# Performance work log

Hardware: AMD Instinct MI355X
Metric: run time of the kernel (lower is better)

The kernel has to match this reference:

```python
import jax, jax.numpy as jnp
import numpy as np

# module hyperparameters (from init_kwargs)
STRIDE, PAD, DIL = 1, 1, 1
GROUPS, DG = 1, 1
KH, KW = 3, 3
CIN, COUT = 256, 256


def _mdcn_forward(x, offset, mask, weight, bias):
    B, C, H, W = x.shape
    Cout = weight.shape[0]
    K = KH * KW
    Ho = (H + 2 * PAD - (DIL * (KH - 1) + 1)) // STRIDE + 1
    Wo = (W + 2 * PAD - (DIL * (KW - 1) + 1)) // STRIDE + 1
    Cg = C // DG

    # offset channel layout: ((g*K + k)*2 + {0: dy, 1: dx})
    off = offset.reshape(B, DG, KH, KW, 2, Ho, Wo)
    base_y = (jnp.arange(Ho) * STRIDE - PAD)[None, :] + DIL * jnp.arange(KH)[:, None]  # [KH,Ho]
    base_x = (jnp.arange(Wo) * STRIDE - PAD)[None, :] + DIL * jnp.arange(KW)[:, None]  # [KW,Wo]
    sy = base_y[None, None, :, None, :, None].astype(x.dtype) + off[:, :, :, :, 0]  # [B,DG,KH,KW,Ho,Wo]
    sx = base_x[None, None, None, :, None, :].astype(x.dtype) + off[:, :, :, :, 1]

    y0f = jnp.floor(sy); x0f = jnp.floor(sx)
    wy = sy - y0f; wx = sx - x0f
    y0 = y0f.astype(jnp.int32); x0 = x0f.astype(jnp.int32)

    xg = x.reshape(B, DG, Cg, H * W)

    def corner(yc, xc, w):
        valid = (yc >= 0) & (yc < H) & (xc >= 0) & (xc < W)
        idx = jnp.clip(yc, 0, H - 1) * W + jnp.clip(xc, 0, W - 1)  # [B,DG,KH,KW,Ho,Wo]
        v = jnp.take_along_axis(xg, idx.reshape(B, DG, 1, -1), axis=3)  # [B,DG,Cg,K*Ho*Wo]
        v = v.reshape(B, DG, Cg, KH, KW, Ho, Wo)
        return v * (w * valid.astype(x.dtype))[:, :, None]

    val = (corner(y0, x0, (1 - wy) * (1 - wx))
           + corner(y0, x0 + 1, (1 - wy) * wx)
           + corner(y0 + 1, x0, wy * (1 - wx))
           + corner(y0 + 1, x0 + 1, wy * wx))  # [B,DG,Cg,KH,KW,Ho,Wo]

    cols = val * mask.reshape(B, DG, 1, KH, KW, Ho, Wo)
    cols = cols.reshape(B, GROUPS, (C // GROUPS) * K, Ho * Wo)
    wg = weight.reshape(GROUPS, Cout // GROUPS, (C // GROUPS) * K)
    out = jnp.einsum('gok,bgkp->bgop', wg, cols).reshape(B, Cout, Ho, Wo)
    return out + bias[None, :, None, None]


def setup_inputs() -> dict:
    key = jax.random.key(0)
    k1, k2, k3, k4 = jax.random.split(key, 4)
    B, H, W = 4, 64, 64
    x = jax.random.normal(k1, (B, CIN, H, W), dtype=jnp.float32)
    offset = jax.random.normal(k2, (B, 2 * DG * KH * KW, H, W), dtype=jnp.float32)
    mask = jax.random.uniform(k3, (B, DG * KH * KW, H, W), dtype=jnp.float32)
    stdv = 1.0 / np.sqrt(CIN * KH * KW)
    weight = jax.random.uniform(k4, (COUT, CIN // GROUPS, KH, KW), dtype=jnp.float32,
                                minval=-stdv, maxval=stdv)
    bias = jnp.zeros((COUT,), dtype=jnp.float32)
    return {"x": x, "offset": offset, "mask": mask, "weight": weight, "bias": bias}


def reference(x, offset, mask, weight, bias):
    return _mdcn_forward(x, offset, mask, weight, bias)
```

## Files before the change

kernel.cpp:

```cpp
#include <hip/hip_runtime.h>
#include <hip/hip_bf16.h>
#include <stdint.h>

#define KDIM 2304

typedef __bf16 bf16_t;
typedef bf16_t bf16x8 __attribute__((ext_vector_type(8)));
typedef float f32x4 __attribute__((ext_vector_type(4)));
typedef float f32x2 __attribute__((ext_vector_type(2)));

__device__ __forceinline__ float b2f_lo(uint32_t u) {
  union { uint32_t i; float f; } c; c.i = u << 16; return c.f;
}
__device__ __forceinline__ float b2f_hi(uint32_t u) {
  union { uint32_t i; float f; } c; c.i = u & 0xffff0000u; return c.f;
}
__device__ __forceinline__ uint32_t pk_bf16(float a, float b) {
  __hip_bfloat162 h = __float22bfloat162_rn(make_float2(a, b));
  union { __hip_bfloat162 h; uint32_t u; } c; c.h = h; return c.u;
}

__device__ __forceinline__ void g2lds16(const uint16_t* g, uint16_t* l) {
  __builtin_amdgcn_global_load_lds((const __attribute__((address_space(1))) void*)g,
                                   (__attribute__((address_space(3))) void*)l,
                                   16, 0, 0);
}

__global__ __launch_bounds__(256) void k_transpose(const float* __restrict__ x,
                                                   uint16_t* __restrict__ xt) {
  __shared__ float tile[32][33];
  int b = blockIdx.z;
  int c0 = blockIdx.y << 5;
  int s0 = blockIdx.x << 5;
  int tid = threadIdx.x;
  int tx = tid & 31, ty = tid >> 5;
  const float* src = x + ((size_t)(b * 256 + c0)) * 4096 + s0;
#pragma unroll
  for (int i = 0; i < 4; ++i)
    tile[ty + i * 8][tx] = src[(size_t)(ty + i * 8) * 4096 + tx];
  __syncthreads();
  int cg = tid & 7, sp = tid >> 3;
  uint2 o;
  o.x = pk_bf16(tile[cg * 4 + 0][sp], tile[cg * 4 + 1][sp]);
  o.y = pk_bf16(tile[cg * 4 + 2][sp], tile[cg * 4 + 3][sp]);
  *(uint2*)&xt[((size_t)b * 4096 + s0 + sp) * 256 + c0 + cg * 4] = o;
}

__global__ __launch_bounds__(256) void k_wprep(const float* __restrict__ w,
                                               uint16_t* __restrict__ wt) {
  int t = blockIdx.x * 256 + threadIdx.x;
  int cout = t / KDIM;
  int r = t - cout * KDIM;
  int k = r >> 8, c = r & 255;
  wt[t] = (uint16_t)(pk_bf16(w[((size_t)(cout * 256 + c)) * 9 + k], 0.f) & 0xffffu);
}

#define BM 128
#define BN 64
#define BK 32
__global__ __launch_bounds__(256) void k_fused(const uint16_t* __restrict__ xt,
                                               const uint16_t* __restrict__ A,
                                               const float* __restrict__ off,
                                               const float* __restrict__ msk,
                                               const float* __restrict__ bias,
                                               float* __restrict__ out) {
  __shared__ __align__(16) uint16_t As[BM * BK];
  __shared__ __align__(16) uint16_t Bs[BN * BK];
  __shared__ float s_off[18 * 64];
  __shared__ float s_msk[9 * 64];

  int tid = threadIdx.x;
  int n0 = blockIdx.x << 6;
  int m0 = blockIdx.y << 7;
  int b = blockIdx.x >> 6;
  int ho = blockIdx.x & 63;

  const float* offb = off + (size_t)b * 18 * 4096 + ho * 64;
  for (int i = tid; i < 18 * 64; i += 256)
    s_off[i] = offb[(size_t)(i >> 6) * 4096 + (i & 63)];
  const float* mskb = msk + (size_t)b * 9 * 4096 + ho * 64;
  for (int i = tid; i < 9 * 64; i += 256)
    s_msk[i] = mskb[(size_t)(i >> 6) * 4096 + (i & 63)];
  __syncthreads();

  int lane = tid & 63, wv = tid >> 6;
  int wm = wv >> 1, wn = wv & 1;
  int q = lane >> 4, r = lane & 15;

  f32x4 acc[4][2];
#pragma unroll
  for (int i = 0; i < 4; ++i)
#pragma unroll
    for (int j = 0; j < 2; ++j) acc[i][j] = f32x4{0.f, 0.f, 0.f, 0.f};

  const uint16_t* a0p = A + (size_t)(m0 + (tid >> 2)) * KDIM + (tid & 3) * 8;
  const uint16_t* a1p = A + (size_t)(m0 + 64 + (tid >> 2)) * KDIM + (tid & 3) * 8;
  uint16_t* as0 = &As[tid * 8];
  uint16_t* as1 = &As[2048 + tid * 8];

  int p = tid >> 2, cq = tid & 3;
  uint16_t* bs_dst = &Bs[tid * 8];
  const uint16_t* xtb = xt + (size_t)b * 4096 * 256 + cq * 8;

  for (int tap = 0; tap < 9; ++tap) {
    int kh = tap / 3, kw = tap - kh * 3;
    float dy = s_off[(2 * tap) * 64 + p];
    float dx = s_off[(2 * tap + 1) * 64 + p];
    float mm = s_msk[tap * 64 + p];
    float sy = (float)(ho - 1 + kh) + dy;
    float sx = (float)(p - 1 + kw) + dx;
    float fy = floorf(sy), fx = floorf(sx);
    int y0 = (int)fy, x0 = (int)fx;
    float wy = sy - fy, wx = sx - fx;
    float cw[4];
    const uint16_t* cp[4];
#pragma unroll
    for (int cy = 0; cy < 2; ++cy) {
#pragma unroll
      for (int cx = 0; cx < 2; ++cx) {
        int y = y0 + cy, x = x0 + cx;
        float w = (cy ? wy : 1.f - wy) * (cx ? wx : 1.f - wx) * mm;
        bool v = ((unsigned)y < 64u) && ((unsigned)x < 64u);
        w = v ? w : 0.f;
        int yc = min(max(y, 0), 63), xc = min(max(x, 0), 63);
        cw[cy * 2 + cx] = w;
        cp[cy * 2 + cx] = xtb + ((yc << 6) + xc) * 256;
      }
    }
    const uint16_t* abase0 = a0p + tap * 256;
    const uint16_t* abase1 = a1p + tap * 256;
#pragma unroll
    for (int st = 0; st < 8; ++st) {
      g2lds16(abase0 + st * 32, as0);
      g2lds16(abase1 + st * 32, as1);
      const uint4 d0 = *(const uint4*)(cp[0] + st * 32);
      const uint4 d1 = *(const uint4*)(cp[1] + st * 32);
      const uint4 d2 = *(const uint4*)(cp[2] + st * 32);
      const uint4 d3 = *(const uint4*)(cp[3] + st * 32);
      f32x2 v0 = {0.f, 0.f}, v1 = {0.f, 0.f}, v2 = {0.f, 0.f}, v3 = {0.f, 0.f};
      f32x2 w0 = {cw[0], cw[0]}, w1 = {cw[1], cw[1]}, w2 = {cw[2], cw[2]}, w3 = {cw[3], cw[3]};
      v0 += w0 * f32x2{b2f_lo(d0.x), b2f_hi(d0.x)};
      v1 += w0 * f32x2{b2f_lo(d0.y), b2f_hi(d0.y)};
      v2 += w0 * f32x2{b2f_lo(d0.z), b2f_hi(d0.z)};
      v3 += w0 * f32x2{b2f_lo(d0.w), b2f_hi(d0.w)};
      v0 += w1 * f32x2{b2f_lo(d1.x), b2f_hi(d1.x)};
      v1 += w1 * f32x2{b2f_lo(d1.y), b2f_hi(d1.y)};
      v2 += w1 * f32x2{b2f_lo(d1.z), b2f_hi(d1.z)};
      v3 += w1 * f32x2{b2f_lo(d1.w), b2f_hi(d1.w)};
      v0 += w2 * f32x2{b2f_lo(d2.x), b2f_hi(d2.x)};
      v1 += w2 * f32x2{b2f_lo(d2.y), b2f_hi(d2.y)};
      v2 += w2 * f32x2{b2f_lo(d2.z), b2f_hi(d2.z)};
      v3 += w2 * f32x2{b2f_lo(d2.w), b2f_hi(d2.w)};
      v0 += w3 * f32x2{b2f_lo(d3.x), b2f_hi(d3.x)};
      v1 += w3 * f32x2{b2f_lo(d3.y), b2f_hi(d3.y)};
      v2 += w3 * f32x2{b2f_lo(d3.z), b2f_hi(d3.z)};
      v3 += w3 * f32x2{b2f_lo(d3.w), b2f_hi(d3.w)};
      uint4 o;
      o.x = pk_bf16(v0.x, v0.y);
      o.y = pk_bf16(v1.x, v1.y);
      o.z = pk_bf16(v2.x, v2.y);
      o.w = pk_bf16(v3.x, v3.y);
      *(uint4*)bs_dst = o;
      __syncthreads();
      bf16x8 af[4], bfr[2];
#pragma unroll
      for (int mi = 0; mi < 4; ++mi)
        af[mi] = *(const bf16x8*)&As[(wm * 64 + mi * 16 + r) * BK + q * 8];
#pragma unroll
      for (int ni = 0; ni < 2; ++ni)
        bfr[ni] = *(const bf16x8*)&Bs[(wn * 32 + ni * 16 + r) * BK + q * 8];
#pragma unroll
      for (int mi = 0; mi < 4; ++mi)
#pragma unroll
        for (int ni = 0; ni < 2; ++ni)
          acc[mi][ni] = __builtin_amdgcn_mfma_f32_16x16x32_bf16(af[mi], bfr[ni], acc[mi][ni], 0, 0, 0);
      __syncthreads();
    }
  }

#pragma unroll
  for (int mi = 0; mi < 4; ++mi) {
#pragma unroll
    for (int j = 0; j < 4; ++j) {
      int m = m0 + wm * 64 + mi * 16 + q * 4 + j;
      float bv = bias[m];
#pragma unroll
      for (int ni = 0; ni < 2; ++ni) {
        int n = n0 + wn * 32 + ni * 16 + r;
        int bb = n >> 12, pp = n & 4095;
        out[((size_t)(bb * 256 + m)) * 4096 + pp] = acc[mi][ni][j] + bv;
      }
    }
  }
}

extern "C" void kernel_launch(void* const* d_in, const int* in_sizes, int n_in,
                              void* d_out, int out_size, void* d_ws, size_t ws_size,
                              hipStream_t stream) {
  (void)in_sizes; (void)n_in; (void)out_size; (void)ws_size;
  const float* x      = (const float*)d_in[0];
  const float* offset = (const float*)d_in[1];
  const float* mask   = (const float*)d_in[2];
  const float* weight = (const float*)d_in[3];
  const float* bias   = (const float*)d_in[4];
  float* out = (float*)d_out;

  uint8_t* ws = (uint8_t*)d_ws;
  uint16_t* xt = (uint16_t*)ws;
  uint16_t* wt = (uint16_t*)(ws + 8388608);

  k_transpose<<<dim3(128, 8, 4), 256, 0, stream>>>(x, xt);
  k_wprep<<<dim3(2304), 256, 0, stream>>>(weight, wt);
  k_fused<<<dim3(256, 2), 256, 0, stream>>>(xt, wt, offset, mask, bias, out);
}
```

Baseline: 142.5 us.

## Merge prep kernels and enlarge fused GEMM tile to 128x128 with K=128 stages

After: 178.8 us. 25.5% more time.

```diff
diff --git a/kernel.cpp b/kernel.cpp
--- a/kernel.cpp
+++ b/kernel.cpp
@@ -26,89 +26,98 @@
                                    16, 0, 0);
 }
 
-__global__ __launch_bounds__(256) void k_transpose(const float* __restrict__ x,
-                                                   uint16_t* __restrict__ xt) {
-  __shared__ float tile[32][33];
-  int b = blockIdx.z;
-  int c0 = blockIdx.y << 5;
-  int s0 = blockIdx.x << 5;
+__global__ __launch_bounds__(256) void k_prep(const float* __restrict__ x,
+                                              uint16_t* __restrict__ xt,
+                                              const float* __restrict__ w,
+                                              uint16_t* __restrict__ wt) {
   int tid = threadIdx.x;
-  int tx = tid & 31, ty = tid >> 5;
-  const float* src = x + ((size_t)(b * 256 + c0)) * 4096 + s0;
-#pragma unroll
-  for (int i = 0; i < 4; ++i)
-    tile[ty + i * 8][tx] = src[(size_t)(ty + i * 8) * 4096 + tx];
-  __syncthreads();
-  int cg = tid & 7, sp = tid >> 3;
-  uint2 o;
-  o.x = pk_bf16(tile[cg * 4 + 0][sp], tile[cg * 4 + 1][sp]);
-  o.y = pk_bf16(tile[cg * 4 + 2][sp], tile[cg * 4 + 3][sp]);
-  *(uint2*)&xt[((size_t)b * 4096 + s0 + sp) * 256 + c0 + cg * 4] = o;
-}
-
-__global__ __launch_bounds__(256) void k_wprep(const float* __restrict__ w,
-                                               uint16_t* __restrict__ wt) {
-  int t = blockIdx.x * 256 + threadIdx.x;
-  int cout = t / KDIM;
-  int r = t - cout * KDIM;
-  int k = r >> 8, c = r & 255;
-  wt[t] = (uint16_t)(pk_bf16(w[((size_t)(cout * 256 + c)) * 9 + k], 0.f) & 0xffffu);
-}
-
-#define BM 128
-#define BN 64
-#define BK 32
-__global__ __launch_bounds__(256) void k_fused(const uint16_t* __restrict__ xt,
-                                               const uint16_t* __restrict__ A,
-                                               const float* __restrict__ off,
-                                               const float* __restrict__ msk,
-                                               const float* __restrict__ bias,
-                                               float* __restrict__ out) {
-  __shared__ __align__(16) uint16_t As[BM * BK];
-  __shared__ __align__(16) uint16_t Bs[BN * BK];
-  __shared__ float s_off[18 * 64];
-  __shared__ float s_msk[9 * 64];
+  if (blockIdx.x < 2048) {
+    __shared__ float tile[32][65];
+    int b = blockIdx.x >> 9;
+    int cgrp = (blockIdx.x >> 6) & 7;
+    int sgrp = blockIdx.x & 63;
+    int c0 = cgrp << 5, s0 = sgrp << 6;
+#pragma unroll
+    for (int it = 0; it < 2; ++it) {
+      int f = tid + it * 256;
+      int r = f >> 4, col = (f & 15) << 2;
+      float4 v = *(const float4*)&x[((size_t)(b * 256 + c0 + r)) * 4096 + s0 + col];
+      tile[r][col + 0] = v.x;
+      tile[r][col + 1] = v.y;
+      tile[r][col + 2] = v.z;
+      tile[r][col + 3] = v.w;
+    }
+    __syncthreads();
+    int sp = tid >> 2, cg = tid & 3;
+    uint4 o;
+    o.x = pk_bf16(tile[cg * 8 + 0][sp], tile[cg * 8 + 1][sp]);
+    o.y = pk_bf16(tile[cg * 8 + 2][sp], tile[cg * 8 + 3][sp]);
+    o.z = pk_bf16(tile[cg * 8 + 4][sp], tile[cg * 8 + 5][sp]);
+    o.w = pk_bf16(tile[cg * 8 + 6][sp], tile[cg * 8 + 7][sp]);
+    *(uint4*)&xt[((size_t)b * 4096 + s0 + sp) * 256 + c0 + cg * 8] = o;
+  } else {
+    __shared__ float wl[2304];
+    int cout = blockIdx.x - 2048;
+    const float* wrow = w + (size_t)cout * 2304;
+    for (int i = tid; i < 576; i += 256)
+      *(float4*)&wl[i * 4] = *(const float4*)&wrow[i * 4];
+    __syncthreads();
+    uint16_t* wdst = wt + (size_t)cout * KDIM + tid;
+#pragma unroll
+    for (int t = 0; t < 9; ++t)
+      wdst[t * 256] = (uint16_t)(pk_bf16(wl[tid * 9 + t], 0.f) & 0xffffu);
+  }
+}
+
+__global__ __launch_bounds__(256, 1) void k_fused(const uint16_t* __restrict__ xt,
+                                                  const uint16_t* __restrict__ wt,
+                                                  const float* __restrict__ off,
+                                                  const float* __restrict__ msk,
+                                                  const float* __restrict__ bias,
+                                                  float* __restrict__ out) {
+  __shared__ __align__(16) uint16_t As[4][128][32];
+  __shared__ __align__(16) uint16_t Bs[4][128][32];
+  __shared__ float s_off[18 * 128];
+  __shared__ float s_msk[9 * 128];
 
   int tid = threadIdx.x;
-  int n0 = blockIdx.x << 6;
+  int b = blockIdx.x >> 5;
+  int hobase = (blockIdx.x & 31) << 1;
+  int n0 = b * 4096 + hobase * 64;
   int m0 = blockIdx.y << 7;
-  int b = blockIdx.x >> 6;
-  int ho = blockIdx.x & 63;
-
-  const float* offb = off + (size_t)b * 18 * 4096 + ho * 64;
-  for (int i = tid; i < 18 * 64; i += 256)
-    s_off[i] = offb[(size_t)(i >> 6) * 4096 + (i & 63)];
-  const float* mskb = msk + (size_t)b * 9 * 4096 + ho * 64;
-  for (int i = tid; i < 9 * 64; i += 256)
-    s_msk[i] = mskb[(size_t)(i >> 6) * 4096 + (i & 63)];
+
+  const float* offb = off + (size_t)b * 18 * 4096 + hobase * 64;
+  for (int i = tid; i < 18 * 128; i += 256)
+    s_off[i] = offb[(size_t)(i >> 7) * 4096 + (i & 127)];
+  const float* mskb = msk + (size_t)b * 9 * 4096 + hobase * 64;
+  for (int i = tid; i < 9 * 128; i += 256)
+    s_msk[i] = mskb[(size_t)(i >> 7) * 4096 + (i & 127)];
   __syncthreads();
 
   int lane = tid & 63, wv = tid >> 6;
   int wm = wv >> 1, wn = wv & 1;
   int q = lane >> 4, r = lane & 15;
 
-  f32x4 acc[4][2];
+  f32x4 acc[4][4];
 #pragma unroll
   for (int i = 0; i < 4; ++i)
 #pragma unroll
-    for (int j = 0; j < 2; ++j) acc[i][j] = f32x4{0.f, 0.f, 0.f, 0.f};
-
-  const uint16_t* a0p = A + (size_t)(m0 + (tid >> 2)) * KDIM + (tid & 3) * 8;
-  const uint16_t* a1p = A + (size_t)(m0 + 64 + (tid >> 2)) * KDIM + (tid & 3) * 8;
-  uint16_t* as0 = &As[tid * 8];
-  uint16_t* as1 = &As[2048 + tid * 8];
-
-  int p = tid >> 2, cq = tid & 3;
-  uint16_t* bs_dst = &Bs[tid * 8];
-  const uint16_t* xtb = xt + (size_t)b * 4096 * 256 + cq * 8;
+    for (int j = 0; j < 4; ++j) acc[i][j] = f32x4{0.f, 0.f, 0.f, 0.f};
+
+  const uint16_t* aptr = wt + (size_t)(m0 + (lane >> 2)) * KDIM + wv * 32 + (lane & 3) * 8;
+
+  int p = tid >> 1, half = tid & 1;
+  const uint16_t* xtb = xt + (size_t)b * 4096 * 256 + half * 64;
+  int ho_p = hobase + (p >> 6);
+  int wo_p = p & 63;
 
   for (int tap = 0; tap < 9; ++tap) {
     int kh = tap / 3, kw = tap - kh * 3;
-    float dy = s_off[(2 * tap) * 64 + p];
-    float dx = s_off[(2 * tap + 1) * 64 + p];
-    float mm = s_msk[tap * 64 + p];
-    float sy = (float)(ho - 1 + kh) + dy;
-    float sx = (float)(p - 1 + kw) + dx;
+    float dy = s_off[(2 * tap) * 128 + p];
+    float dx = s_off[(2 * tap + 1) * 128 + p];
+    float mm = s_msk[tap * 128 + p];
+    float sy = (float)(ho_p - 1 + kh) + dy;
+    float sx = (float)(wo_p - 1 + kw) + dx;
     float fy = floorf(sy), fx = floorf(sx);
     int y0 = (int)fy, x0 = (int)fx;
     float wy = sy - fy, wx = sx - fx;
@@ -118,62 +127,66 @@
     for (int cy = 0; cy < 2; ++cy) {
 #pragma unroll
       for (int cx = 0; cx < 2; ++cx) {
-        int y = y0 + cy, x = x0 + cx;
-        float w = (cy ? wy : 1.f - wy) * (cx ? wx : 1.f - wx) * mm;
-        bool v = ((unsigned)y < 64u) && ((unsigned)x < 64u);
-        w = v ? w : 0.f;
-        int yc = min(max(y, 0), 63), xc = min(max(x, 0), 63);
-        cw[cy * 2 + cx] = w;
+        int y = y0 + cy, xx = x0 + cx;
+        float wgt = (cy ? wy : 1.f - wy) * (cx ? wx : 1.f - wx) * mm;
+        bool v = ((unsigned)y < 64u) && ((unsigned)xx < 64u);
+        wgt = v ? wgt : 0.f;
+        int yc = min(max(y, 0), 63), xc = min(max(xx, 0), 63);
+        cw[cy * 2 + cx] = wgt;
         cp[cy * 2 + cx] = xtb + ((yc << 6) + xc) * 256;
       }
     }
-    const uint16_t* abase0 = a0p + tap * 256;
-    const uint16_t* abase1 = a1p + tap * 256;
-#pragma unroll
-    for (int st = 0; st < 8; ++st) {
-      g2lds16(abase0 + st * 32, as0);
-      g2lds16(abase1 + st * 32, as1);
-      const uint4 d0 = *(const uint4*)(cp[0] + st * 32);
-      const uint4 d1 = *(const uint4*)(cp[1] + st * 32);
-      const uint4 d2 = *(const uint4*)(cp[2] + st * 32);
-      const uint4 d3 = *(const uint4*)(cp[3] + st * 32);
-      f32x2 v0 = {0.f, 0.f}, v1 = {0.f, 0.f}, v2 = {0.f, 0.f}, v3 = {0.f, 0.f};
-      f32x2 w0 = {cw[0], cw[0]}, w1 = {cw[1], cw[1]}, w2 = {cw[2], cw[2]}, w3 = {cw[3], cw[3]};
-      v0 += w0 * f32x2{b2f_lo(d0.x), b2f_hi(d0.x)};
-      v1 += w0 * f32x2{b2f_lo(d0.y), b2f_hi(d0.y)};
-      v2 += w0 * f32x2{b2f_lo(d0.z), b2f_hi(d0.z)};
-      v3 += w0 * f32x2{b2f_lo(d0.w), b2f_hi(d0.w)};
-      v0 += w1 * f32x2{b2f_lo(d1.x), b2f_hi(d1.x)};
-      v1 += w1 * f32x2{b2f_lo(d1.y), b2f_hi(d1.y)};
-      v2 += w1 * f32x2{b2f_lo(d1.z), b2f_hi(d1.z)};
-      v3 += w1 * f32x2{b2f_lo(d1.w), b2f_hi(d1.w)};
-      v0 += w2 * f32x2{b2f_lo(d2.x), b2f_hi(d2.x)};
-      v1 += w2 * f32x2{b2f_lo(d2.y), b2f_hi(d2.y)};
-      v2 += w2 * f32x2{b2f_lo(d2.z), b2f_hi(d2.z)};
-      v3 += w2 * f32x2{b2f_lo(d2.w), b2f_hi(d2.w)};
-      v0 += w3 * f32x2{b2f_lo(d3.x), b2f_hi(d3.x)};
-      v1 += w3 * f32x2{b2f_lo(d3.y), b2f_hi(d3.y)};
-      v2 += w3 * f32x2{b2f_lo(d3.z), b2f_hi(d3.z)};
-      v3 += w3 * f32x2{b2f_lo(d3.w), b2f_hi(d3.w)};
-      uint4 o;
-      o.x = pk_bf16(v0.x, v0.y);
-      o.y = pk_bf16(v1.x, v1.y);
-      o.z = pk_bf16(v2.x, v2.y);
-      o.w = pk_bf16(v3.x, v3.y);
-      *(uint4*)bs_dst = o;
+    const uint16_t* atap = aptr + tap * 256;
+#pragma unroll
+    for (int ht = 0; ht < 2; ++ht) {
+#pragma unroll
+      for (int j = 0; j < 8; ++j)
+        g2lds16(atap + ht * 128 + (size_t)j * 16 * KDIM, &As[wv][j * 16][0]);
+      int choff = ht * 128;
+      f32x2 facc[32];
+#pragma unroll
+      for (int u = 0; u < 32; ++u) facc[u] = f32x2{0.f, 0.f};
+#pragma unroll
+      for (int c = 0; c < 4; ++c) {
+        const uint4* src = (const uint4*)(cp[c] + choff);
+        uint4 d[8];
+#pragma unroll
+        for (int u = 0; u < 8; ++u) d[u] = src[u];
+        f32x2 wc = {cw[c], cw[c]};
+#pragma unroll
+        for (int u = 0; u < 8; ++u) {
+          facc[u * 4 + 0] += wc * f32x2{b2f_lo(d[u].x), b2f_hi(d[u].x)};
+          facc[u * 4 + 1] += wc * f32x2{b2f_lo(d[u].y), b2f_hi(d[u].y)};
+          facc[u * 4 + 2] += wc * f32x2{b2f_lo(d[u].z), b2f_hi(d[u].z)};
+          facc[u * 4 + 3] += wc * f32x2{b2f_lo(d[u].w), b2f_hi(d[u].w)};
+        }
+      }
+#pragma unroll
+      for (int cc = 0; cc < 8; ++cc) {
+        uint4 o;
+        o.x = pk_bf16(facc[cc * 4 + 0].x, facc[cc * 4 + 0].y);
+        o.y = pk_bf16(facc[cc * 4 + 1].x, facc[cc * 4 + 1].y);
+        o.z = pk_bf16(facc[cc * 4 + 2].x, facc[cc * 4 + 2].y);
+        o.w = pk_bf16(facc[cc * 4 + 3].x, facc[cc * 4 + 3].y);
+        int st = half * 2 + (cc >> 2);
+        *(uint4*)&Bs[st][p][(cc & 3) * 8] = o;
+      }
       __syncthreads();
-      bf16x8 af[4], bfr[2];
-#pragma unroll
-      for (int mi = 0; mi < 4; ++mi)
-        af[mi] = *(const bf16x8*)&As[(wm * 64 + mi * 16 + r) * BK + q * 8];
-#pragma unroll
-      for (int ni = 0; ni < 2; ++ni)
-        bfr[ni] = *(const bf16x8*)&Bs[(wn * 32 + ni * 16 + r) * BK + q * 8];
-#pragma unroll
-      for (int mi = 0; mi < 4; ++mi)
-#pragma unroll
-        for (int ni = 0; ni < 2; ++ni)
-          acc[mi][ni] = __builtin_amdgcn_mfma_f32_16x16x32_bf16(af[mi], bfr[ni], acc[mi][ni], 0, 0, 0);
+#pragma unroll
+      for (int st = 0; st < 4; ++st) {
+        bf16x8 af[4], bf[4];
+#pragma unroll
+        for (int mi = 0; mi < 4; ++mi)
+          af[mi] = *(const bf16x8*)&As[st][wm * 64 + mi * 16 + r][q * 8];
+#pragma unroll
+        for (int ni = 0; ni < 4; ++ni)
+          bf[ni] = *(const bf16x8*)&Bs[st][wn * 64 + ni * 16 + r][q * 8];
+#pragma unroll
+        for (int mi = 0; mi < 4; ++mi)
+#pragma unroll
+          for (int ni = 0; ni < 4; ++ni)
+            acc[mi][ni] = __builtin_amdgcn_mfma_f32_16x16x32_bf16(af[mi], bf[ni], acc[mi][ni], 0, 0, 0);
+      }
       __syncthreads();
     }
   }
@@ -185,8 +198,8 @@
       int m = m0 + wm * 64 + mi * 16 + q * 4 + j;
       float bv = bias[m];
 #pragma unroll
-      for (int ni = 0; ni < 2; ++ni) {
-        int n = n0 + wn * 32 + ni * 16 + r;
+      for (int ni = 0; ni < 4; ++ni) {
+        int n = n0 + wn * 64 + ni * 16 + r;
         int bb = n >> 12, pp = n & 4095;
         out[((size_t)(bb * 256 + m)) * 4096 + pp] = acc[mi][ni][j] + bv;
       }
@@ -209,7 +222,6 @@
   uint16_t* xt = (uint16_t*)ws;
   uint16_t* wt = (uint16_t*)(ws + 8388608);
 
-  k_transpose<<<dim3(128, 8, 4), 256, 0, stream>>>(x, xt);
-  k_wprep<<<dim3(2304), 256, 0, stream>>>(weight, wt);
-  k_fused<<<dim3(256, 2), 256, 0, stream>>>(xt, wt, offset, mask, bias, out);
-}
+  k_prep<<<dim3(2304), 256, 0, stream>>>(x, xt, weight, wt);
+  k_fused<<<dim3(128, 2), 256, 0, stream>>>(xt, wt, offset, mask, bias, out);
+}
```
